# Kernel optimization log

Measured on AMD Instinct MI355X. Metric: run time of the kernel, lower is better.

The kernel has to match this reference:

```python
import jax, jax.numpy as jnp
import numpy as np

N_NODES = 50000
HIDDEN = 128
N_EDGES = 800000


def gcn_conv(x, edge_index, W, b):
    # PyG GCNConv: h = x @ W (no bias); add self-loops; symmetric norm; scatter-add; + bias
    h = x @ W  # [N, H]
    row, col = edge_index[0], edge_index[1]
    sl = jnp.arange(N_NODES)
    row_f = jnp.concatenate([row, sl])
    col_f = jnp.concatenate([col, sl])
    ones = jnp.ones(row_f.shape[0], dtype=x.dtype)
    deg = jax.ops.segment_sum(ones, col_f, num_segments=N_NODES)  # in-degree incl self-loop
    dinv = jnp.where(deg > 0, jax.lax.rsqrt(deg), 0.0)
    norm = dinv[row_f] * dinv[col_f]  # [E+N]
    msgs = h[row_f] * norm[:, None]   # gather + scale
    out = jax.ops.segment_sum(msgs, col_f, num_segments=N_NODES)  # scatter-add
    return out + b


def setup_inputs() -> dict:
    key = jax.random.key(0)
    ks = jax.random.split(key, 12)
    H = HIDDEN
    s = 1.0 / np.sqrt(H)
    x = jax.random.normal(ks[0], (N_NODES, H), dtype=jnp.float32)
    edge_index = jax.random.randint(ks[1], (2, N_EDGES), 0, N_NODES, dtype=jnp.int64)
    W1 = jax.random.uniform(ks[2], (H, H), jnp.float32, -s, s)
    b1 = jax.random.uniform(ks[3], (H,), jnp.float32, -s, s)
    W2 = jax.random.uniform(ks[4], (H, H), jnp.float32, -s, s)
    b2 = jax.random.uniform(ks[5], (H,), jnp.float32, -s, s)
    s2 = 1.0 / np.sqrt(2 * H)
    We1 = jax.random.uniform(ks[6], (2 * H, H), jnp.float32, -s2, s2)
    be1 = jax.random.uniform(ks[7], (H,), jnp.float32, -s2, s2)
    We2 = jax.random.uniform(ks[8], (H, 1), jnp.float32, -s, s)
    be2 = jax.random.uniform(ks[9], (1,), jnp.float32, -s, s)
    return {"x": x, "edge_index": edge_index, "W1": W1, "b1": b1, "W2": W2,
            "b2": b2, "We1": We1, "be1": be1, "We2": We2, "be2": be2}


def reference(x, edge_index, W1, b1, W2, b2, We1, be1, We2, be2):
    h = jax.nn.relu(gcn_conv(x, edge_index, W1, b1))
    h = jax.nn.relu(gcn_conv(h, edge_index, W2, b2))
    row, col = edge_index[0], edge_index[1]
    ef = jnp.concatenate([h[row], h[col]], axis=1)  # [E, 2H]
    z = jax.nn.relu(ef @ We1 + be1)
    p = jax.nn.sigmoid(z @ We2 + be2)  # [E, 1]
    return p.squeeze(-1)
```

## Files before the change

kernel.cpp:

```cpp
#include <hip/hip_runtime.h>
#include <math.h>

#define NND 50000
#define HD  128
#define NE  800000
#define NBK 196
#define BINB 391
#define NCH 391

typedef unsigned short u16;
typedef unsigned int   u32;
typedef __attribute__((ext_vector_type(8))) short bf16x8;
typedef __attribute__((ext_vector_type(4))) float f32x4;

__device__ __forceinline__ float bf2f(u32 u) {
  union { u32 i; float f; } v; v.i = u << 16; return v.f;
}
__device__ __forceinline__ u16 f2bf(float f) {
  union { float f; u32 i; } v; v.f = f;
  return (u16)((v.i + 0x7FFFu + ((v.i >> 16) & 1u)) >> 16);
}
__device__ __forceinline__ void unpack8(uint4 m, float* f) {
  f[0] = bf2f(m.x & 0xFFFFu); f[1] = bf2f(m.x >> 16);
  f[2] = bf2f(m.y & 0xFFFFu); f[3] = bf2f(m.y >> 16);
  f[4] = bf2f(m.z & 0xFFFFu); f[5] = bf2f(m.z >> 16);
  f[6] = bf2f(m.w & 0xFFFFu); f[7] = bf2f(m.w >> 16);
}

__global__ __launch_bounds__(256) void k_prep(const int* __restrict__ col, u32* __restrict__ bhist,
                                              const float* __restrict__ W1, const float* __restrict__ W2,
                                              const float* __restrict__ We1,
                                              u16* __restrict__ t1h, u16* __restrict__ t1l,
                                              u16* __restrict__ t2h, u16* __restrict__ t2l,
                                              u16* __restrict__ teh, u16* __restrict__ tel) {
  __shared__ u32 lh[NBK];
  int tid = threadIdx.x;
  if (blockIdx.x < BINB) {
    if (tid < NBK) lh[tid] = 0;
    __syncthreads();
    int e0 = blockIdx.x * 2048;
    #pragma unroll
    for (int s = 0; s < 8; ++s) {
      int e = e0 + s * 256 + tid;
      if (e < NE) atomicAdd(&lh[col[e] >> 8], 1u);
    }
    __syncthreads();
    if (tid < NBK && lh[tid]) atomicAdd(&bhist[tid], lh[tid]);
    return;
  }
  int idx = (blockIdx.x - BINB) * 256 + tid;
  float w;
  u16 *dh, *dl;
  int j;
  if (idx < 16384) {
    j = idx; int n = j >> 7, k = j & 127;
    w = W1[k * 128 + n]; dh = t1h; dl = t1l;
  } else if (idx < 32768) {
    j = idx - 16384; int n = j >> 7, k = j & 127;
    w = W2[k * 128 + n]; dh = t2h; dl = t2l;
  } else {
    j = idx - 32768; int n = j >> 7, k = j & 127;
    w = (n < 128) ? We1[k * 128 + n] : We1[(128 + k) * 128 + (n - 128)];
    dh = teh; dl = tel;
  }
  int n = j >> 7, k = j & 127;
  int sidx = n * 128 + ((((k >> 3) ^ (n & 7))) << 3) + (k & 7);
  u16 hi = f2bf(w);
  float res = w - bf2f((u32)hi);
  dh[sidx] = hi;
  dl[sidx] = f2bf(res);
}

__global__ __launch_bounds__(256) void k_bscan(const u32* __restrict__ bhist, u32* __restrict__ bbase,
                                               u32* __restrict__ bcur) {
  __shared__ u32 ws[4];
  int tid = threadIdx.x, lane = tid & 63, wid = tid >> 6;
  u32 d = (tid < NBK) ? bhist[tid] : 0;
  u32 x = d;
  #pragma unroll
  for (int off = 1; off < 64; off <<= 1) {
    u32 y = __shfl_up(x, off);
    if (lane >= off) x += y;
  }
  if (lane == 63) ws[wid] = x;
  __syncthreads();
  u32 woff = 0;
  for (int w = 0; w < wid; ++w) woff += ws[w];
  if (tid < NBK) { bbase[tid] = woff + x - d; bcur[tid] = woff + x - d; }
}

__global__ __launch_bounds__(256) void k_bin(const int* __restrict__ row, const int* __restrict__ col,
                                             u32* __restrict__ bcur, uint2* __restrict__ recs) {
  __shared__ u32 lcount[NBK], lbase[NBK];
  int tid = threadIdx.x;
  if (tid < NBK) lcount[tid] = 0;
  __syncthreads();
  int e0 = blockIdx.x * 2048;
  u32 rank[8]; int cv[8];
  #pragma unroll
  for (int s = 0; s < 8; ++s) {
    int e = e0 + s * 256 + tid;
    if (e < NE) {
      cv[s] = col[e];
      rank[s] = atomicAdd(&lcount[cv[s] >> 8], 1u);
    }
  }
  __syncthreads();
  if (tid < NBK && lcount[tid]) lbase[tid] = atomicAdd(&bcur[tid], lcount[tid]);
  __syncthreads();
  #pragma unroll
  for (int s = 0; s < 8; ++s) {
    int e = e0 + s * 256 + tid;
    if (e < NE) {
      int c = cv[s];
      u32 slot = lbase[c >> 8] + rank[s];
      recs[slot] = make_uint2((u32)row[e] | (((u32)c & 255u) << 16), (u32)e);
    }
  }
}

__global__ __launch_bounds__(256) void k_fine(const u32* __restrict__ bhist, const u32* __restrict__ bbase,
                                              const uint2* __restrict__ recs, uint2* __restrict__ sre,
                                              int* __restrict__ ptr, float* __restrict__ dinv) {
  __shared__ u32 lh[256];
  __shared__ u32 ws[4];
  int b = blockIdx.x, tid = threadIdx.x, lane = tid & 63, wid = tid >> 6;
  u32 base = bbase[b], cnt = bhist[b];
  lh[tid] = 0;
  __syncthreads();
  for (u32 i = tid; i < cnt; i += 256) atomicAdd(&lh[(recs[base + i].x >> 16) & 255u], 1u);
  __syncthreads();
  u32 ci = lh[tid];
  u32 x = ci;
  #pragma unroll
  for (int off = 1; off < 64; off <<= 1) {
    u32 y = __shfl_up(x, off);
    if (lane >= off) x += y;
  }
  if (lane == 63) ws[wid] = x;
  __syncthreads();
  u32 woff = 0;
  for (int w = 0; w < wid; ++w) woff += ws[w];
  u32 excl = woff + x - ci;
  int node = b * 256 + tid;
  if (node <= NND) ptr[node] = (int)(base + excl);
  if (node < NND) dinv[node] = rsqrtf((float)(ci + 1));
  __syncthreads();
  lh[tid] = excl;
  __syncthreads();
  for (u32 i = tid; i < cnt; i += 256) {
    uint2 rec = recs[base + i];
    u32 r = atomicAdd(&lh[(rec.x >> 16) & 255u], 1u);
    sre[base + r] = make_uint2(rec.x & 0xFFFFu, rec.y);
  }
}

__device__ __forceinline__ void mm_body(const void* Xv, bool afp32,
                                        const u16* Whi, const u16* Wlo,
                                        u16* OUT, const float* scale, int ostride) {
  __shared__ __align__(16) u16 Bh[128 * 128];
  __shared__ __align__(16) u16 Bl[128 * 128];
  int tid = threadIdx.x;
  int h = blockIdx.x / NCH;
  int chunk = blockIdx.x - h * NCH;
  Whi += (size_t)h * 128 * 128;
  Wlo += (size_t)h * 128 * 128;
  int ooff = h * 128;
  {
    const uint4* gh = (const uint4*)Whi;
    const uint4* gl = (const uint4*)Wlo;
    uint4* lh = (uint4*)Bh;
    uint4* ll = (uint4*)Bl;
    #pragma unroll
    for (int i = 0; i < 4; ++i) {
      lh[tid + i * 512] = gh[tid + i * 512];
      ll[tid + i * 512] = gl[tid + i * 512];
    }
  }
  __syncthreads();
  int wid = tid >> 6, lane = tid & 63;
  int m16 = lane & 15, kg = lane >> 4;
  int arow = chunk * 128 + wid * 16 + m16;
  int ar = (arow < NND) ? arow : NND - 1;
  bf16x8 afrag[4];
  if (afp32) {
    const float* X = (const float*)Xv + (size_t)ar * 128 + kg * 8;
    #pragma unroll
    for (int ks = 0; ks < 4; ++ks) {
      float4 a = *(const float4*)(X + ks * 32);
      float4 b = *(const float4*)(X + ks * 32 + 4);
      union { u32 w[4]; bf16x8 v; } u;
      u.w[0] = (u32)f2bf(a.x) | ((u32)f2bf(a.y) << 16);
      u.w[1] = (u32)f2bf(a.z) | ((u32)f2bf(a.w) << 16);
      u.w[2] = (u32)f2bf(b.x) | ((u32)f2bf(b.y) << 16);
      u.w[3] = (u32)f2bf(b.z) | ((u32)f2bf(b.w) << 16);
      afrag[ks] = u.v;
    }
  } else {
    const u16* X = (const u16*)Xv + (size_t)ar * 128 + kg * 8;
    #pragma unroll
    for (int ks = 0; ks < 4; ++ks) afrag[ks] = *(const bf16x8*)(X + ks * 32);
  }
  int crow0 = chunk * 128 + wid * 16 + kg * 4;
  float sc[4];
  #pragma unroll
  for (int j = 0; j < 4; ++j)
    sc[j] = (scale != nullptr && crow0 + j < NND) ? scale[crow0 + j] : 1.0f;
  #pragma unroll
  for (int t = 0; t < 8; ++t) {
    int coln = t * 16 + m16;
    f32x4 acc = {0.f, 0.f, 0.f, 0.f};
    #pragma unroll
    for (int ks = 0; ks < 4; ++ks) {
      int c8 = (ks * 4 + kg) ^ (coln & 7);
      bf16x8 bhf = *(const bf16x8*)(Bh + coln * 128 + c8 * 8);
      bf16x8 blf = *(const bf16x8*)(Bl + coln * 128 + c8 * 8);
      acc = __builtin_amdgcn_mfma_f32_16x16x32_bf16(afrag[ks], bhf, acc, 0, 0, 0);
      acc = __builtin_amdgcn_mfma_f32_16x16x32_bf16(afrag[ks], blf, acc, 0, 0, 0);
    }
    #pragma unroll
    for (int j = 0; j < 4; ++j) {
      int r = crow0 + j;
      if (r < NND) OUT[(size_t)r * ostride + ooff + coln] = f2bf(acc[j] * sc[j]);
    }
  }
}

template<bool AFP32>
__global__ __launch_bounds__(512) void k_mm(const void* __restrict__ Xv,
                                            const u16* __restrict__ Whi, const u16* __restrict__ Wlo,
                                            u16* __restrict__ OUT, const float* __restrict__ scale,
                                            int ostride) {
  mm_body(Xv, AFP32, Whi, Wlo, OUT, scale, ostride);
}

__global__ __launch_bounds__(256) void k_gather(const int* __restrict__ ptr, const uint2* __restrict__ sre,
                                                const float* __restrict__ dinv, const u16* __restrict__ Ts,
                                                u16* __restrict__ H, const float* __restrict__ bias) {
  int wid = threadIdx.x >> 6, lane = threadIdx.x & 63;
  int ch8 = lane & 15, slot = lane >> 4;
  int v = blockIdx.x * 4 + wid; if (v >= NND) return;
  int p0 = ptr[v], p1 = ptr[v + 1];
  const uint4* T4 = (const uint4*)Ts;
  float acc[8];
  if (slot == 0) {
    uint4 m = T4[(size_t)v * 16 + ch8];
    unpack8(m, acc);
  } else {
    #pragma unroll
    for (int k = 0; k < 8; ++k) acc[k] = 0.f;
  }
  for (int j2 = p0; j2 < p1; j2 += 32) {
    bool ok[8]; int r[8];
    #pragma unroll
    for (int u = 0; u < 8; ++u) {
      int j = j2 + u * 4 + slot;
      ok[u] = j < p1;
      r[u] = (int)sre[ok[u] ? j : p0].x;
    }
    uint4 m[8];
    #pragma unroll
    for (int u = 0; u < 8; ++u) m[u] = T4[(size_t)r[u] * 16 + ch8];
    #pragma unroll
    for (int u = 0; u < 8; ++u) {
      if (ok[u]) {
        float f[8]; unpack8(m[u], f);
        #pragma unroll
        for (int k = 0; k < 8; ++k) acc[k] += f[k];
      }
    }
  }
  #pragma unroll
  for (int k = 0; k < 8; ++k) {
    acc[k] += __shfl_xor(acc[k], 16);
    acc[k] += __shfl_xor(acc[k], 32);
  }
  if (slot == 0) {
    float s = dinv[v];
    float4 ba = *(const float4*)(bias + ch8 * 8);
    float4 bb = *(const float4*)(bias + ch8 * 8 + 4);
    float bv[8] = {ba.x, ba.y, ba.z, ba.w, bb.x, bb.y, bb.z, bb.w};
    u32 pk[4];
    #pragma unroll
    for (int k = 0; k < 4; ++k) {
      float o0 = fmaxf(fmaf(acc[2 * k], s, bv[2 * k]), 0.f);
      float o1 = fmaxf(fmaf(acc[2 * k + 1], s, bv[2 * k + 1]), 0.f);
      pk[k] = (u32)f2bf(o0) | ((u32)f2bf(o1) << 16);
    }
    *(uint4*)(H + (size_t)v * 128 + ch8 * 8) = make_uint4(pk[0], pk[1], pk[2], pk[3]);
  }
}

__global__ __launch_bounds__(256) void k_edge(const int* __restrict__ ptr, const uint2* __restrict__ sre,
                                              const u16* __restrict__ UV,
                                              const float* __restrict__ be1, const float* __restrict__ We2,
                                              const float* __restrict__ be2, float* __restrict__ out) {
  int wid = threadIdx.x >> 6, lane = threadIdx.x & 63;
  int ch8 = lane & 15, slot = lane >> 4;
  int c = blockIdx.x * 4 + wid; if (c >= NND) return;
  int p0 = ptr[c], p1 = ptr[c + 1];
  if (p0 == p1) return;
  const uint4* UV4 = (const uint4*)UV;
  float vv[8];
  {
    uint4 mv = UV4[(size_t)c * 32 + 16 + ch8];
    unpack8(mv, vv);
    float4 ba = *(const float4*)(be1 + ch8 * 8);
    float4 bb = *(const float4*)(be1 + ch8 * 8 + 4);
    vv[0] += ba.x; vv[1] += ba.y; vv[2] += ba.z; vv[3] += ba.w;
    vv[4] += bb.x; vv[5] += bb.y; vv[6] += bb.z; vv[7] += bb.w;
  }
  float w2[8];
  {
    float4 wa = *(const float4*)(We2 + ch8 * 8);
    float4 wb = *(const float4*)(We2 + ch8 * 8 + 4);
    w2[0] = wa.x; w2[1] = wa.y; w2[2] = wa.z; w2[3] = wa.w;
    w2[4] = wb.x; w2[5] = wb.y; w2[6] = wb.z; w2[7] = wb.w;
  }
  float bias2 = be2[0];
  for (int j2 = p0; j2 < p1; j2 += 32) {
    bool ok[8]; uint2 e[8];
    #pragma unroll
    for (int u = 0; u < 8; ++u) {
      int j = j2 + u * 4 + slot;
      ok[u] = j < p1;
      e[u] = sre[ok[u] ? j : p0];
    }
    uint4 m[8];
    #pragma unroll
    for (int u = 0; u < 8; ++u) m[u] = UV4[(size_t)e[u].x * 32 + ch8];
    float p[8];
    #pragma unroll
    for (int u = 0; u < 8; ++u) {
      float f[8]; unpack8(m[u], f);
      float s0 = fmaxf(f[0] + vv[0], 0.f) * w2[0] + fmaxf(f[1] + vv[1], 0.f) * w2[1];
      s0 += fmaxf(f[2] + vv[2], 0.f) * w2[2] + fmaxf(f[3] + vv[3], 0.f) * w2[3];
      s0 += fmaxf(f[4] + vv[4], 0.f) * w2[4] + fmaxf(f[5] + vv[5], 0.f) * w2[5];
      s0 += fmaxf(f[6] + vv[6], 0.f) * w2[6] + fmaxf(f[7] + vv[7], 0.f) * w2[7];
      p[u] = s0;
    }
    #pragma unroll
    for (int off = 8; off; off >>= 1) {
      #pragma unroll
      for (int u = 0; u < 8; ++u) p[u] += __shfl_xor(p[u], off);
    }
    if (ch8 == 0) {
      #pragma unroll
      for (int u = 0; u < 8; ++u)
        if (ok[u]) out[e[u].y] = 1.f / (1.f + __expf(-(p[u] + bias2)));
    }
  }
}

extern "C" void kernel_launch(void* const* d_in, const int* in_sizes, int n_in,
                              void* d_out, int out_size, void* d_ws, size_t ws_size,
                              hipStream_t stream) {
  const float* x   = (const float*)d_in[0];
  const int*   ei  = (const int*)d_in[1];
  const float* W1  = (const float*)d_in[2];
  const float* b1  = (const float*)d_in[3];
  const float* W2  = (const float*)d_in[4];
  const float* b2  = (const float*)d_in[5];
  const float* We1 = (const float*)d_in[6];
  const float* be1 = (const float*)d_in[7];
  const float* We2 = (const float*)d_in[8];
  const float* be2 = (const float*)d_in[9];
  float* out = (float*)d_out;

  const int* row  = ei;
  const int* colp = ei + NE;

  if (ws_size < (size_t)16166240 * 4) return;
  int*   ptr    = (int*)d_ws;
  float* dinv   = (float*)d_ws + 50064;
  u32*   bhist  = (u32*)d_ws + 100112;
  u32*   bbase  = (u32*)d_ws + 100308;
  u32*   bcur   = (u32*)d_ws + 100504;
  uint2* recs   = (uint2*)((u32*)d_ws + 100704);
  uint2* sre    = (uint2*)((u32*)d_ws + 1700704);
  u16*   t1h    = (u16*)((u32*)d_ws + 3300704);
  u16*   t1l    = (u16*)((u32*)d_ws + 3308896);
  u16*   t2h    = (u16*)((u32*)d_ws + 3317088);
  u16*   t2l    = (u16*)((u32*)d_ws + 3325280);
  u16*   teh    = (u16*)((u32*)d_ws + 3333472);
  u16*   tel    = (u16*)((u32*)d_ws + 3349856);
  u16*   Ts     = (u16*)((u32*)d_ws + 3366240);
  u16*   H      = (u16*)((u32*)d_ws + 6566240);
  u16*   UV     = (u16*)((u32*)d_ws + 9766240);

  (void)hipMemsetAsync(bhist, 0, NBK * sizeof(u32), stream);
  k_prep <<<BINB + 256, 256, 0, stream>>>(colp, bhist, W1, W2, We1, t1h, t1l, t2h, t2l, teh, tel);
  k_bscan<<<1, 256, 0, stream>>>(bhist, bbase, bcur);
  k_bin  <<<BINB, 256, 0, stream>>>(row, colp, bcur, recs);
  k_fine <<<NBK, 256, 0, stream>>>(bhist, bbase, recs, sre, ptr, dinv);

  int node_grid = (NND + 3) / 4;

  k_mm<true><<<NCH, 512, 0, stream>>>(x, t1h, t1l, Ts, dinv, 128);
  k_gather<<<node_grid, 256, 0, stream>>>(ptr, sre, dinv, Ts, H, b1);

  k_mm<false><<<NCH, 512, 0, stream>>>(H, t2h, t2l, Ts, dinv, 128);
  k_gather<<<node_grid, 256, 0, stream>>>(ptr, sre, dinv, Ts, H, b2);

  k_mm<false><<<2 * NCH, 512, 0, stream>>>(H, teh, tel, UV, nullptr, 256);
  k_edge<<<node_grid, 256, 0, stream>>>(ptr, sre, UV, be1, We2, be2, out);
}
```

Baseline: 199.5 us.

## Degree-sort nodes for gather and make edge kernel edge-parallel

Adds a degree histogram, scan and placement pass that builds a node permutation, so each gather wave processes nodes of similar in-degree to reduce load imbalance. The edge MLP kernel becomes edge-parallel with a fixed 32 edges per wave, reading the destination node from high bits packed into the sorted edge records instead of walking per-node CSR ranges. The be1 bias is folded into the third matmul's epilogue. This costs two extra small launches and atomics, and gather now reads nodes in scattered order.

```diff
diff --git a/kernel.cpp b/kernel.cpp
--- a/kernel.cpp
+++ b/kernel.cpp
@@ -121,7 +121,8 @@
 
 __global__ __launch_bounds__(256) void k_fine(const u32* __restrict__ bhist, const u32* __restrict__ bbase,
                                               const uint2* __restrict__ recs, uint2* __restrict__ sre,
-                                              int* __restrict__ ptr, float* __restrict__ dinv) {
+                                              int* __restrict__ ptr, float* __restrict__ dinv,
+                                              u32* __restrict__ dhist) {
   __shared__ u32 lh[256];
   __shared__ u32 ws[4];
   int b = blockIdx.x, tid = threadIdx.x, lane = tid & 63, wid = tid >> 6;
@@ -144,20 +145,47 @@
   u32 excl = woff + x - ci;
   int node = b * 256 + tid;
   if (node <= NND) ptr[node] = (int)(base + excl);
-  if (node < NND) dinv[node] = rsqrtf((float)(ci + 1));
+  if (node < NND) {
+    dinv[node] = rsqrtf((float)(ci + 1));
+    atomicAdd(&dhist[ci < 63u ? ci : 63u], 1u);
+  }
   __syncthreads();
   lh[tid] = excl;
   __syncthreads();
   for (u32 i = tid; i < cnt; i += 256) {
     uint2 rec = recs[base + i];
-    u32 r = atomicAdd(&lh[(rec.x >> 16) & 255u], 1u);
-    sre[base + r] = make_uint2(rec.x & 0xFFFFu, rec.y);
-  }
+    u32 cidx = (rec.x >> 16) & 255u;
+    u32 r = atomicAdd(&lh[cidx], 1u);
+    sre[base + r] = make_uint2((rec.x & 0xFFFFu) | (((u32)b * 256u + cidx) << 16), rec.y);
+  }
+}
+
+__global__ __launch_bounds__(64) void k_dscan(const u32* __restrict__ dhist, u32* __restrict__ dcur) {
+  int lane = threadIdx.x;
+  u32 d = dhist[lane];
+  u32 x = d;
+  #pragma unroll
+  for (int off = 1; off < 64; off <<= 1) {
+    u32 y = __shfl_down(x, off);
+    if (lane + off < 64) x += y;
+  }
+  dcur[lane] = x - d;
+}
+
+__global__ __launch_bounds__(256) void k_dplace(const int* __restrict__ ptr, u32* __restrict__ dcur,
+                                                int* __restrict__ perm) {
+  int v = blockIdx.x * 256 + threadIdx.x;
+  if (v >= NND) return;
+  int d = ptr[v + 1] - ptr[v];
+  int b = d < 63 ? d : 63;
+  u32 slot = atomicAdd(&dcur[b], 1u);
+  perm[slot] = v;
 }
 
 __device__ __forceinline__ void mm_body(const void* Xv, bool afp32,
                                         const u16* Whi, const u16* Wlo,
-                                        u16* OUT, const float* scale, int ostride) {
+                                        u16* OUT, const float* scale, int ostride,
+                                        const float* bias) {
   __shared__ __align__(16) u16 Bh[128 * 128];
   __shared__ __align__(16) u16 Bl[128 * 128];
   int tid = threadIdx.x;
@@ -209,6 +237,7 @@
   #pragma unroll
   for (int t = 0; t < 8; ++t) {
     int coln = t * 16 + m16;
+    float badd = (bias != nullptr && h != 0) ? bias[coln] : 0.f;
     f32x4 acc = {0.f, 0.f, 0.f, 0.f};
     #pragma unroll
     for (int ks = 0; ks < 4; ++ks) {
@@ -221,7 +250,7 @@
     #pragma unroll
     for (int j = 0; j < 4; ++j) {
       int r = crow0 + j;
-      if (r < NND) OUT[(size_t)r * ostride + ooff + coln] = f2bf(acc[j] * sc[j]);
+      if (r < NND) OUT[(size_t)r * ostride + ooff + coln] = f2bf(acc[j] * sc[j] + badd);
     }
   }
 }
@@ -230,16 +259,18 @@
 __global__ __launch_bounds__(512) void k_mm(const void* __restrict__ Xv,
                                             const u16* __restrict__ Whi, const u16* __restrict__ Wlo,
                                             u16* __restrict__ OUT, const float* __restrict__ scale,
-                                            int ostride) {
-  mm_body(Xv, AFP32, Whi, Wlo, OUT, scale, ostride);
+                                            int ostride, const float* __restrict__ bias) {
+  mm_body(Xv, AFP32, Whi, Wlo, OUT, scale, ostride, bias);
 }
 
 __global__ __launch_bounds__(256) void k_gather(const int* __restrict__ ptr, const uint2* __restrict__ sre,
+                                                const int* __restrict__ perm,
                                                 const float* __restrict__ dinv, const u16* __restrict__ Ts,
                                                 u16* __restrict__ H, const float* __restrict__ bias) {
   int wid = threadIdx.x >> 6, lane = threadIdx.x & 63;
   int ch8 = lane & 15, slot = lane >> 4;
-  int v = blockIdx.x * 4 + wid; if (v >= NND) return;
+  int idx = blockIdx.x * 4 + wid; if (idx >= NND) return;
+  int v = perm[idx];
   int p0 = ptr[v], p1 = ptr[v + 1];
   const uint4* T4 = (const uint4*)Ts;
   float acc[8];
@@ -256,7 +287,7 @@
     for (int u = 0; u < 8; ++u) {
       int j = j2 + u * 4 + slot;
       ok[u] = j < p1;
-      r[u] = (int)sre[ok[u] ? j : p0].x;
+      r[u] = (int)(sre[ok[u] ? j : p0].x & 0xFFFFu);
     }
     uint4 m[8];
     #pragma unroll
@@ -291,25 +322,14 @@
   }
 }
 
-__global__ __launch_bounds__(256) void k_edge(const int* __restrict__ ptr, const uint2* __restrict__ sre,
+__global__ __launch_bounds__(256) void k_edge(const uint2* __restrict__ sre,
                                               const u16* __restrict__ UV,
-                                              const float* __restrict__ be1, const float* __restrict__ We2,
+                                              const float* __restrict__ We2,
                                               const float* __restrict__ be2, float* __restrict__ out) {
   int wid = threadIdx.x >> 6, lane = threadIdx.x & 63;
   int ch8 = lane & 15, slot = lane >> 4;
-  int c = blockIdx.x * 4 + wid; if (c >= NND) return;
-  int p0 = ptr[c], p1 = ptr[c + 1];
-  if (p0 == p1) return;
+  int e0 = (blockIdx.x * 4 + wid) * 32;
   const uint4* UV4 = (const uint4*)UV;
-  float vv[8];
-  {
-    uint4 mv = UV4[(size_t)c * 32 + 16 + ch8];
-    unpack8(mv, vv);
-    float4 ba = *(const float4*)(be1 + ch8 * 8);
-    float4 bb = *(const float4*)(be1 + ch8 * 8 + 4);
-    vv[0] += ba.x; vv[1] += ba.y; vv[2] += ba.z; vv[3] += ba.w;
-    vv[4] += bb.x; vv[5] += bb.y; vv[6] += bb.z; vv[7] += bb.w;
-  }
   float w2[8];
   {
     float4 wa = *(const float4*)(We2 + ch8 * 8);
@@ -318,37 +338,39 @@
     w2[4] = wb.x; w2[5] = wb.y; w2[6] = wb.z; w2[7] = wb.w;
   }
   float bias2 = be2[0];
-  for (int j2 = p0; j2 < p1; j2 += 32) {
-    bool ok[8]; uint2 e[8];
-    #pragma unroll
-    for (int u = 0; u < 8; ++u) {
-      int j = j2 + u * 4 + slot;
-      ok[u] = j < p1;
-      e[u] = sre[ok[u] ? j : p0];
-    }
-    uint4 m[8];
-    #pragma unroll
-    for (int u = 0; u < 8; ++u) m[u] = UV4[(size_t)e[u].x * 32 + ch8];
-    float p[8];
-    #pragma unroll
-    for (int u = 0; u < 8; ++u) {
-      float f[8]; unpack8(m[u], f);
-      float s0 = fmaxf(f[0] + vv[0], 0.f) * w2[0] + fmaxf(f[1] + vv[1], 0.f) * w2[1];
-      s0 += fmaxf(f[2] + vv[2], 0.f) * w2[2] + fmaxf(f[3] + vv[3], 0.f) * w2[3];
-      s0 += fmaxf(f[4] + vv[4], 0.f) * w2[4] + fmaxf(f[5] + vv[5], 0.f) * w2[5];
-      s0 += fmaxf(f[6] + vv[6], 0.f) * w2[6] + fmaxf(f[7] + vv[7], 0.f) * w2[7];
-      p[u] = s0;
-    }
-    #pragma unroll
-    for (int off = 8; off; off >>= 1) {
-      #pragma unroll
-      for (int u = 0; u < 8; ++u) p[u] += __shfl_xor(p[u], off);
-    }
-    if (ch8 == 0) {
-      #pragma unroll
-      for (int u = 0; u < 8; ++u)
-        if (ok[u]) out[e[u].y] = 1.f / (1.f + __expf(-(p[u] + bias2)));
-    }
+  uint2 e[8];
+  #pragma unroll
+  for (int u = 0; u < 8; ++u) e[u] = sre[e0 + u * 4 + slot];
+  uint4 m[8];
+  #pragma unroll
+  for (int u = 0; u < 8; ++u) m[u] = UV4[(size_t)(e[u].x & 0xFFFFu) * 32 + ch8];
+  float p[8];
+  float vv[8];
+  int ccur = -1;
+  #pragma unroll
+  for (int u = 0; u < 8; ++u) {
+    int c = (int)(e[u].x >> 16);
+    if (c != ccur) {
+      uint4 mv = UV4[(size_t)c * 32 + 16 + ch8];
+      unpack8(mv, vv);
+      ccur = c;
+    }
+    float f[8]; unpack8(m[u], f);
+    float s0 = fmaxf(f[0] + vv[0], 0.f) * w2[0] + fmaxf(f[1] + vv[1], 0.f) * w2[1];
+    s0 += fmaxf(f[2] + vv[2], 0.f) * w2[2] + fmaxf(f[3] + vv[3], 0.f) * w2[3];
+    s0 += fmaxf(f[4] + vv[4], 0.f) * w2[4] + fmaxf(f[5] + vv[5], 0.f) * w2[5];
+    s0 += fmaxf(f[6] + vv[6], 0.f) * w2[6] + fmaxf(f[7] + vv[7], 0.f) * w2[7];
+    p[u] = s0;
+  }
+  #pragma unroll
+  for (int off = 8; off; off >>= 1) {
+    #pragma unroll
+    for (int u = 0; u < 8; ++u) p[u] += __shfl_xor(p[u], off);
+  }
+  if (ch8 == 0) {
+    #pragma unroll
+    for (int u = 0; u < 8; ++u)
+      out[e[u].y] = 1.f / (1.f + __expf(-(p[u] + bias2)));
   }
 }
 
@@ -370,38 +392,44 @@
   const int* row  = ei;
   const int* colp = ei + NE;
 
-  if (ws_size < (size_t)16166240 * 4) return;
+  if (ws_size < (size_t)16216364 * 4) return;
   int*   ptr    = (int*)d_ws;
   float* dinv   = (float*)d_ws + 50064;
   u32*   bhist  = (u32*)d_ws + 100112;
-  u32*   bbase  = (u32*)d_ws + 100308;
-  u32*   bcur   = (u32*)d_ws + 100504;
-  uint2* recs   = (uint2*)((u32*)d_ws + 100704);
-  uint2* sre    = (uint2*)((u32*)d_ws + 1700704);
-  u16*   t1h    = (u16*)((u32*)d_ws + 3300704);
-  u16*   t1l    = (u16*)((u32*)d_ws + 3308896);
-  u16*   t2h    = (u16*)((u32*)d_ws + 3317088);
-  u16*   t2l    = (u16*)((u32*)d_ws + 3325280);
-  u16*   teh    = (u16*)((u32*)d_ws + 3333472);
-  u16*   tel    = (u16*)((u32*)d_ws + 3349856);
-  u16*   Ts     = (u16*)((u32*)d_ws + 3366240);
-  u16*   H      = (u16*)((u32*)d_ws + 6566240);
-  u16*   UV     = (u16*)((u32*)d_ws + 9766240);
-
-  (void)hipMemsetAsync(bhist, 0, NBK * sizeof(u32), stream);
-  k_prep <<<BINB + 256, 256, 0, stream>>>(colp, bhist, W1, W2, We1, t1h, t1l, t2h, t2l, teh, tel);
-  k_bscan<<<1, 256, 0, stream>>>(bhist, bbase, bcur);
-  k_bin  <<<BINB, 256, 0, stream>>>(row, colp, bcur, recs);
-  k_fine <<<NBK, 256, 0, stream>>>(bhist, bbase, recs, sre, ptr, dinv);
+  u32*   dhist  = (u32*)d_ws + 100308;
+  u32*   dcur   = (u32*)d_ws + 100372;
+  u32*   bbase  = (u32*)d_ws + 100436;
+  u32*   bcur   = (u32*)d_ws + 100632;
+  int*   perm   = (int*)d_ws + 100828;
+  uint2* recs   = (uint2*)((u32*)d_ws + 150828);
+  uint2* sre    = (uint2*)((u32*)d_ws + 1750828);
+  u16*   t1h    = (u16*)((u32*)d_ws + 3350828);
+  u16*   t1l    = (u16*)((u32*)d_ws + 3359020);
+  u16*   t2h    = (u16*)((u32*)d_ws + 3367212);
+  u16*   t2l    = (u16*)((u32*)d_ws + 3375404);
+  u16*   teh    = (u16*)((u32*)d_ws + 3383596);
+  u16*   tel    = (u16*)((u32*)d_ws + 3399980);
+  u16*   Ts     = (u16*)((u32*)d_ws + 3416364);
+  u16*   H      = (u16*)((u32*)d_ws + 6616364);
+  u16*   UV     = (u16*)((u32*)d_ws + 9816364);
+
+  (void)hipMemsetAsync(bhist, 0, (NBK + 64) * sizeof(u32), stream);
+  k_prep  <<<BINB + 256, 256, 0, stream>>>(colp, bhist, W1, W2, We1, t1h, t1l, t2h, t2l, teh, tel);
+  k_bscan <<<1, 256, 0, stream>>>(bhist, bbase, bcur);
+  k_bin   <<<BINB, 256, 0, stream>>>(row, colp, bcur, recs);
+  k_fine  <<<NBK, 256, 0, stream>>>(bhist, bbase, recs, sre, ptr, dinv, dhist);
+  k_dscan <<<1, 64, 0, stream>>>(dhist, dcur);
+  k_dplace<<<NBK, 256, 0, stream>>>(ptr, dcur, perm);
 
   int node_grid = (NND + 3) / 4;
-
-  k_mm<true><<<NCH, 512, 0, stream>>>(x, t1h, t1l, Ts, dinv, 128);
-  k_gather<<<node_grid, 256, 0, stream>>>(ptr, sre, dinv, Ts, H, b1);
-
-  k_mm<false><<<NCH, 512, 0, stream>>>(H, t2h, t2l, Ts, dinv, 128);
-  k_gather<<<node_grid, 256, 0, stream>>>(ptr, sre, dinv, Ts, H, b2);
-
-  k_mm<false><<<2 * NCH, 512, 0, stream>>>(H, teh, tel, UV, nullptr, 256);
-  k_edge<<<node_grid, 256, 0, stream>>>(ptr, sre, UV, be1, We2, be2, out);
-}
+  int edge_grid = NE / 128;
+
+  k_mm<true><<<NCH, 512, 0, stream>>>(x, t1h, t1l, Ts, dinv, 128, nullptr);
+  k_gather<<<node_grid, 256, 0, stream>>>(ptr, sre, perm, dinv, Ts, H, b1);
+
+  k_mm<false><<<NCH, 512, 0, stream>>>(H, t2h, t2l, Ts, dinv, 128, nullptr);
+  k_gather<<<node_grid, 256, 0, stream>>>(ptr, sre, perm, dinv, Ts, H, b2);
+
+  k_mm<false><<<2 * NCH, 512, 0, stream>>>(H, teh, tel, UV, nullptr, 256, be1);
+  k_edge<<<edge_grid, 256, 0, stream>>>(sre, UV, We2, be2, out);
+}
```

Result: slower. 520.3 us (+160.8%).
